# Performance work log

Measured on AMD Instinct MI355X. Metric: run time of the kernel, lower is better.

The kernel has to match this reference:

```python
import jax, jax.numpy as jnp
import numpy as np


def setup_inputs() -> dict:
    key = jax.random.key(0)
    k1, k2 = jax.random.split(key)
    N, D = 8192, 1024
    x = jax.random.normal(k1, (N, D), dtype=jnp.float32)
    w = jax.random.normal(k2, (D, 1), dtype=jnp.float32)
    return {"x": x, "w": w}


def reference(x, w):
    # x: [N, D], w: [D, 1]
    N = x.shape[0]
    a = jax.nn.sigmoid(x @ w)[:, 0]          # [N], values in (0, 1)
    b = jnp.cumsum(a)                         # [N] running sum
    idx = jnp.floor(b).astype(jnp.int32)      # bin index per column
    prev = jnp.concatenate([jnp.zeros(1, jnp.int32), idx[:-1]])
    same = idx == prev                        # did we stay in the same bin?
    frac = b - idx.astype(b.dtype)            # portion falling into bin `idx`
    cols = jnp.arange(N)
    # value written at [idx, i]: a_i if same bin, else the fractional overflow
    main_val = jnp.where(same, a, frac)
    # cross-boundary remainder written at [idx-1, i]
    cross_val = jnp.where(same, 0.0, a - frac)
    cross_row = jnp.where(same, idx, idx - 1)  # dummy (add 0) when same
    trans_mat = (
        jnp.zeros((N, N), dtype=x.dtype)
        .at[idx, cols].set(main_val)
        .at[cross_row, cols].add(cross_val)
    )
    return trans_mat @ x                      # [N, D]
```

## Files before the change

kernel.cpp:

```cpp
#include <hip/hip_runtime.h>
#include <math.h>


__global__ void dot_sigmoid_kernel(const float* __restrict__ x,
                                   const float* __restrict__ w,
                                   float* __restrict__ a, int N, int D) {
  int lane = threadIdx.x & 63;
  int wave = threadIdx.x >> 6;
  int row = blockIdx.x * (blockDim.x >> 6) + wave;
  if (row >= N) return;
  const float4* xr = reinterpret_cast<const float4*>(x + (size_t)row * D);
  const float4* w4 = reinterpret_cast<const float4*>(w);
  float acc = 0.f;
  int nv = D >> 2;
  for (int j = lane; j < nv; j += 64) {
    float4 xv = xr[j];
    float4 wv = w4[j];
    acc = fmaf(xv.x, wv.x, acc);
    acc = fmaf(xv.y, wv.y, acc);
    acc = fmaf(xv.z, wv.z, acc);
    acc = fmaf(xv.w, wv.w, acc);
  }
#pragma unroll
  for (int off = 32; off > 0; off >>= 1) acc += __shfl_down(acc, off, 64);
  if (lane == 0) a[row] = 1.0f / (1.0f + expf(-acc));
}

__global__ __launch_bounds__(1024) void scan_kernel(const float* __restrict__ a,
                                                    float* __restrict__ mainv,
                                                    float* __restrict__ crossv,
                                                    int* __restrict__ rowptr, int N) {
  __shared__ float sa[8192];
  __shared__ double wtot[16];
  __shared__ double woff[16];
  int t = threadIdx.x;
  for (int k = t; k < N; k += 1024) sa[k] = a[k];
  for (int k = t; k <= N; k += 1024) rowptr[k] = N;
  if (t == 0) rowptr[0] = 0;
  __syncthreads();

  int per = N / 1024;
  int base = t * per;
  double loc[8];
  double run = 0.0;
#pragma unroll
  for (int j = 0; j < 8; ++j) {
    run += (double)sa[base + j];
    loc[j] = run;
  }
  double v = run;
  int lane = t & 63;
  int wid = t >> 6;
  for (int off = 1; off < 64; off <<= 1) {
    double n = __shfl_up(v, off, 64);
    if (lane >= off) v += n;
  }
  if (lane == 63) wtot[wid] = v;
  __syncthreads();
  if (t == 0) {
    double s = 0.0;
    for (int k2 = 0; k2 < 16; ++k2) { woff[k2] = s; s += wtot[k2]; }
  }
  __syncthreads();
  double pre = woff[wid] + (v - run);
  double prevbd = pre;
#pragma unroll
  for (int j = 0; j < 8; ++j) {
    int i = base + j;
    double bd = pre + loc[j];
    float bf = (float)bd;
    float pf = (float)prevbd;
    int k = (int)floorf(bf);
    int kp = (int)floorf(pf);
    float ai = sa[i];
    float frac = bf - (float)k;
    bool same = (k == kp);
    mainv[i] = same ? ai : frac;
    crossv[i] = same ? 0.f : (ai - frac);
    if (!same) rowptr[k] = i;
    prevbd = bd;
  }
}

__global__ __launch_bounds__(256) void out_kernel(const float* __restrict__ x,
                                                  const float* __restrict__ mainv,
                                                  const float* __restrict__ crossv,
                                                  const int* __restrict__ rowptr,
                                                  float* __restrict__ out, int N, int D) {
  int r = blockIdx.x;
  int s0 = rowptr[r];
  int s1 = rowptr[r + 1];

  int c = threadIdx.x << 2;
  float4 acc = make_float4(0.f, 0.f, 0.f, 0.f);
  for (int i = s0; i < s1; ++i) {
    float wgt = mainv[i];
    float4 xv = *reinterpret_cast<const float4*>(x + (size_t)i * D + c);
    acc.x = fmaf(wgt, xv.x, acc.x);
    acc.y = fmaf(wgt, xv.y, acc.y);
    acc.z = fmaf(wgt, xv.z, acc.z);
    acc.w = fmaf(wgt, xv.w, acc.w);
  }
  if (s1 < N) {
    float wgt = crossv[s1];
    float4 xv = *reinterpret_cast<const float4*>(x + (size_t)s1 * D + c);
    acc.x = fmaf(wgt, xv.x, acc.x);
    acc.y = fmaf(wgt, xv.y, acc.y);
    acc.z = fmaf(wgt, xv.z, acc.z);
    acc.w = fmaf(wgt, xv.w, acc.w);
  }
  *reinterpret_cast<float4*>(out + (size_t)r * D + c) = acc;
}

extern "C" void kernel_launch(void* const* d_in, const int* in_sizes, int n_in,
                              void* d_out, int out_size, void* d_ws, size_t ws_size,
                              hipStream_t stream) {
  const float* x = (const float*)d_in[0];
  const float* w = (const float*)d_in[1];
  float* out = (float*)d_out;
  int D = in_sizes[1];
  int N = in_sizes[0] / D;

  float* a = (float*)d_ws;
  float* mainv = a + N;
  float* crossv = mainv + N;
  int* rowptr = (int*)(crossv + N);

  int waves_per_block = 4;
  dim3 g1((N + waves_per_block - 1) / waves_per_block);
  hipLaunchKernelGGL(dot_sigmoid_kernel, g1, dim3(256), 0, stream, x, w, a, N, D);

  hipLaunchKernelGGL(scan_kernel, dim3(1), dim3(1024), 0, stream, a, mainv, crossv,
                     rowptr, N);

  hipLaunchKernelGGL(out_kernel, dim3(N), dim3(D / 4), 0, stream, x, mainv, crossv,
                     rowptr, out, N, D);
}
```

Before: 103.0 us.

## Fuse dot-sigmoid with scan via last-block pattern and process two rows per block

Merges the dot-sigmoid and scan kernels into one launch. Each block computes four dot products, and the last block to finish (found with an atomic counter) runs the prefix scan with 256 threads over 32 elements each. The output kernel now handles two rows per block so the shared boundary row of x is loaded once for both rows. It also skips rows whose main weight is below 1e-7. This saves a launch and redundant loads, but adds a memset, a 32KB shared array in every block that can limit occupancy, a longer serial scan per thread, and a small approximation from the skipped weights.

```diff
diff --git a/kernel.cpp b/kernel.cpp
--- a/kernel.cpp
+++ b/kernel.cpp
@@ -2,72 +2,68 @@
 #include <math.h>
 
 
-__global__ void dot_sigmoid_kernel(const float* __restrict__ x,
-                                   const float* __restrict__ w,
-                                   float* __restrict__ a, int N, int D) {
-  int lane = threadIdx.x & 63;
-  int wave = threadIdx.x >> 6;
-  int row = blockIdx.x * (blockDim.x >> 6) + wave;
-  if (row >= N) return;
-  const float4* xr = reinterpret_cast<const float4*>(x + (size_t)row * D);
-  const float4* w4 = reinterpret_cast<const float4*>(w);
-  float acc = 0.f;
-  int nv = D >> 2;
-  for (int j = lane; j < nv; j += 64) {
-    float4 xv = xr[j];
-    float4 wv = w4[j];
-    acc = fmaf(xv.x, wv.x, acc);
-    acc = fmaf(xv.y, wv.y, acc);
-    acc = fmaf(xv.z, wv.z, acc);
-    acc = fmaf(xv.w, wv.w, acc);
+__global__ __launch_bounds__(256) void dot_scan_kernel(
+    const float* __restrict__ x, const float* __restrict__ w,
+    float* __restrict__ a, float* __restrict__ mainv, float* __restrict__ crossv,
+    int* __restrict__ rowptr, int* __restrict__ counter, int N, int D) {
+  __shared__ float sa[8192];
+  __shared__ double wtot[4];
+  __shared__ double woff[4];
+  __shared__ int lastflag;
+  int t = threadIdx.x;
+  int lane = t & 63;
+  int wave = t >> 6;
+
+  int row = blockIdx.x * 4 + wave;
+  {
+    const float4* xr = reinterpret_cast<const float4*>(x + (size_t)row * D);
+    const float4* w4 = reinterpret_cast<const float4*>(w);
+    float acc = 0.f;
+    int nv = D >> 2;
+    for (int j = lane; j < nv; j += 64) {
+      float4 xv = xr[j];
+      float4 wv = w4[j];
+      acc = fmaf(xv.x, wv.x, acc);
+      acc = fmaf(xv.y, wv.y, acc);
+      acc = fmaf(xv.z, wv.z, acc);
+      acc = fmaf(xv.w, wv.w, acc);
+    }
+#pragma unroll
+    for (int off = 32; off > 0; off >>= 1) acc += __shfl_down(acc, off, 64);
+    if (lane == 0) a[row] = 1.0f / (1.0f + expf(-acc));
   }
-#pragma unroll
-  for (int off = 32; off > 0; off >>= 1) acc += __shfl_down(acc, off, 64);
-  if (lane == 0) a[row] = 1.0f / (1.0f + expf(-acc));
-}
+  if (t < 4) rowptr[blockIdx.x * 4 + t] = N;
+  if (blockIdx.x == 0 && t == 4) rowptr[N] = N;
 
-__global__ __launch_bounds__(1024) void scan_kernel(const float* __restrict__ a,
-                                                    float* __restrict__ mainv,
-                                                    float* __restrict__ crossv,
-                                                    int* __restrict__ rowptr, int N) {
-  __shared__ float sa[8192];
-  __shared__ double wtot[16];
-  __shared__ double woff[16];
-  int t = threadIdx.x;
-  for (int k = t; k < N; k += 1024) sa[k] = a[k];
-  for (int k = t; k <= N; k += 1024) rowptr[k] = N;
-  if (t == 0) rowptr[0] = 0;
+  __threadfence();
+  if (t == 0) lastflag = (atomicAdd(counter, 1) == (int)gridDim.x - 1);
   __syncthreads();
+  if (!lastflag) return;
+  __threadfence();
 
-  int per = N / 1024;
+  for (int k = t; k < N; k += 256) sa[k] = a[k];
+  __syncthreads();
+  const int per = N / 256;
   int base = t * per;
-  double loc[8];
   double run = 0.0;
-#pragma unroll
-  for (int j = 0; j < 8; ++j) {
-    run += (double)sa[base + j];
-    loc[j] = run;
-  }
+  for (int j = 0; j < per; ++j) run += (double)sa[base + j];
   double v = run;
-  int lane = t & 63;
-  int wid = t >> 6;
   for (int off = 1; off < 64; off <<= 1) {
     double n = __shfl_up(v, off, 64);
     if (lane >= off) v += n;
   }
-  if (lane == 63) wtot[wid] = v;
+  if (lane == 63) wtot[wave] = v;
   __syncthreads();
   if (t == 0) {
     double s = 0.0;
-    for (int k2 = 0; k2 < 16; ++k2) { woff[k2] = s; s += wtot[k2]; }
+    for (int q = 0; q < 4; ++q) { woff[q] = s; s += wtot[q]; }
   }
   __syncthreads();
-  double pre = woff[wid] + (v - run);
-  double prevbd = pre;
-#pragma unroll
-  for (int j = 0; j < 8; ++j) {
+  double prevbd = woff[wave] + (v - run);
+  if (t == 0) rowptr[0] = 0;
+  for (int j = 0; j < per; ++j) {
     int i = base + j;
-    double bd = pre + loc[j];
+    double bd = prevbd + (double)sa[i];
     float bf = (float)bd;
     float pf = (float)prevbd;
     int k = (int)floorf(bf);
@@ -82,34 +78,60 @@
   }
 }
 
-__global__ __launch_bounds__(256) void out_kernel(const float* __restrict__ x,
-                                                  const float* __restrict__ mainv,
-                                                  const float* __restrict__ crossv,
-                                                  const int* __restrict__ rowptr,
-                                                  float* __restrict__ out, int N, int D) {
-  int r = blockIdx.x;
-  int s0 = rowptr[r];
-  int s1 = rowptr[r + 1];
+__global__ __launch_bounds__(256) void out_kernel(
+    const float* __restrict__ x, const float* __restrict__ mainv,
+    const float* __restrict__ crossv, const int* __restrict__ rowptr,
+    float* __restrict__ out, int N, int D) {
+  int r0 = blockIdx.x * 2;
+  int s0 = rowptr[r0];
+  int s1 = rowptr[r0 + 1];
+  int s2 = rowptr[r0 + 2];
 
   int c = threadIdx.x << 2;
-  float4 acc = make_float4(0.f, 0.f, 0.f, 0.f);
+  float4 acc0 = make_float4(0.f, 0.f, 0.f, 0.f);
+  float4 acc1 = make_float4(0.f, 0.f, 0.f, 0.f);
+
   for (int i = s0; i < s1; ++i) {
     float wgt = mainv[i];
+    if (wgt < 1e-7f) continue;
     float4 xv = *reinterpret_cast<const float4*>(x + (size_t)i * D + c);
-    acc.x = fmaf(wgt, xv.x, acc.x);
-    acc.y = fmaf(wgt, xv.y, acc.y);
-    acc.z = fmaf(wgt, xv.z, acc.z);
-    acc.w = fmaf(wgt, xv.w, acc.w);
+    acc0.x = fmaf(wgt, xv.x, acc0.x);
+    acc0.y = fmaf(wgt, xv.y, acc0.y);
+    acc0.z = fmaf(wgt, xv.z, acc0.z);
+    acc0.w = fmaf(wgt, xv.w, acc0.w);
   }
   if (s1 < N) {
-    float wgt = crossv[s1];
+    float wc = crossv[s1];
+    float wm = mainv[s1];
     float4 xv = *reinterpret_cast<const float4*>(x + (size_t)s1 * D + c);
-    acc.x = fmaf(wgt, xv.x, acc.x);
-    acc.y = fmaf(wgt, xv.y, acc.y);
-    acc.z = fmaf(wgt, xv.z, acc.z);
-    acc.w = fmaf(wgt, xv.w, acc.w);
+    acc0.x = fmaf(wc, xv.x, acc0.x);
+    acc0.y = fmaf(wc, xv.y, acc0.y);
+    acc0.z = fmaf(wc, xv.z, acc0.z);
+    acc0.w = fmaf(wc, xv.w, acc0.w);
+    acc1.x = fmaf(wm, xv.x, acc1.x);
+    acc1.y = fmaf(wm, xv.y, acc1.y);
+    acc1.z = fmaf(wm, xv.z, acc1.z);
+    acc1.w = fmaf(wm, xv.w, acc1.w);
   }
-  *reinterpret_cast<float4*>(out + (size_t)r * D + c) = acc;
+  for (int i = s1 + 1; i < s2; ++i) {
+    float wgt = mainv[i];
+    if (wgt < 1e-7f) continue;
+    float4 xv = *reinterpret_cast<const float4*>(x + (size_t)i * D + c);
+    acc1.x = fmaf(wgt, xv.x, acc1.x);
+    acc1.y = fmaf(wgt, xv.y, acc1.y);
+    acc1.z = fmaf(wgt, xv.z, acc1.z);
+    acc1.w = fmaf(wgt, xv.w, acc1.w);
+  }
+  if (s2 < N) {
+    float wc = crossv[s2];
+    float4 xv = *reinterpret_cast<const float4*>(x + (size_t)s2 * D + c);
+    acc1.x = fmaf(wc, xv.x, acc1.x);
+    acc1.y = fmaf(wc, xv.y, acc1.y);
+    acc1.z = fmaf(wc, xv.z, acc1.z);
+    acc1.w = fmaf(wc, xv.w, acc1.w);
+  }
+  *reinterpret_cast<float4*>(out + (size_t)r0 * D + c) = acc0;
+  *reinterpret_cast<float4*>(out + (size_t)(r0 + 1) * D + c) = acc1;
 }
 
 extern "C" void kernel_launch(void* const* d_in, const int* in_sizes, int n_in,
@@ -125,14 +147,13 @@
   float* mainv = a + N;
   float* crossv = mainv + N;
   int* rowptr = (int*)(crossv + N);
+  int* counter = rowptr + (N + 1);
 
-  int waves_per_block = 4;
-  dim3 g1((N + waves_per_block - 1) / waves_per_block);
-  hipLaunchKernelGGL(dot_sigmoid_kernel, g1, dim3(256), 0, stream, x, w, a, N, D);
+  hipMemsetAsync(counter, 0, sizeof(int), stream);
 
-  hipLaunchKernelGGL(scan_kernel, dim3(1), dim3(1024), 0, stream, a, mainv, crossv,
-                     rowptr, N);
+  hipLaunchKernelGGL(dot_scan_kernel, dim3(N / 4), dim3(256), 0, stream,
+                     x, w, a, mainv, crossv, rowptr, counter, N, D);
 
-  hipLaunchKernelGGL(out_kernel, dim3(N), dim3(D / 4), 0, stream, x, mainv, crossv,
-                     rowptr, out, N, D);
+  hipLaunchKernelGGL(out_kernel, dim3(N / 2), dim3(256), 0, stream,
+                     x, mainv, crossv, rowptr, out, N, D);
 }
```

New measurement: 247.2 us. +140.1%, slower.

## Process eight output rows per block, skipping empty tail rows directly

Applied to the files above, without the earlier changes.

The output kernel now gives each block eight consecutive output rows, walking the contiguous column range once and using a stored per-column bin index to flush finished rows. Rows past the last bin are zero-filled without issuing a block of their own, and the per-column weights are staged in LDS. Blocks whose range is empty or very short, which is most of the bottom half of the grid, now return quickly instead of each launching a separate workgroup. It also skips x loads when the main weight is near zero, which changes results slightly, and adds an extra index array to the workspace.

```diff
diff --git a/kernel.cpp b/kernel.cpp
--- a/kernel.cpp
+++ b/kernel.cpp
@@ -29,6 +29,7 @@
 __global__ __launch_bounds__(1024) void scan_kernel(const float* __restrict__ a,
                                                     float* __restrict__ mainv,
                                                     float* __restrict__ crossv,
+                                                    int* __restrict__ idxv,
                                                     int* __restrict__ rowptr, int N) {
   __shared__ float sa[8192];
   __shared__ double wtot[16];
@@ -39,7 +40,7 @@
   if (t == 0) rowptr[0] = 0;
   __syncthreads();
 
-  int per = N / 1024;
+  const int per = 8;
   int base = t * per;
   double loc[8];
   double run = 0.0;
@@ -59,7 +60,7 @@
   __syncthreads();
   if (t == 0) {
     double s = 0.0;
-    for (int k2 = 0; k2 < 16; ++k2) { woff[k2] = s; s += wtot[k2]; }
+    for (int q = 0; q < 16; ++q) { woff[q] = s; s += wtot[q]; }
   }
   __syncthreads();
   double pre = woff[wid] + (v - run);
@@ -77,39 +78,83 @@
     bool same = (k == kp);
     mainv[i] = same ? ai : frac;
     crossv[i] = same ? 0.f : (ai - frac);
+    idxv[i] = k;
     if (!same) rowptr[k] = i;
     prevbd = bd;
   }
 }
 
-__global__ __launch_bounds__(256) void out_kernel(const float* __restrict__ x,
-                                                  const float* __restrict__ mainv,
-                                                  const float* __restrict__ crossv,
-                                                  const int* __restrict__ rowptr,
-                                                  float* __restrict__ out, int N, int D) {
-  int r = blockIdx.x;
-  int s0 = rowptr[r];
-  int s1 = rowptr[r + 1];
+constexpr int R = 8;
+constexpr int CAP = 1024;
 
-  int c = threadIdx.x << 2;
+__global__ __launch_bounds__(256) void out_kernel(
+    const float* __restrict__ x, const float* __restrict__ mainv,
+    const float* __restrict__ crossv, const int* __restrict__ idxv,
+    const int* __restrict__ rowptr, float* __restrict__ out, int N, int D) {
+  __shared__ float sm[CAP];
+  __shared__ float sc[CAP];
+  __shared__ int sk[CAP];
+  int r0 = blockIdx.x * R;
+  int s_begin = rowptr[r0];
+  int s_endp = rowptr[r0 + R];
+  int len = s_endp - s_begin;
+  int total = len + (s_endp < N ? 1 : 0);
+  int t = threadIdx.x;
+  bool use_lds = (s_begin < N) && (total <= CAP);
+  if (use_lds) {
+    for (int j = t; j < total; j += 256) {
+      sm[j] = mainv[s_begin + j];
+      sc[j] = crossv[s_begin + j];
+      sk[j] = idxv[s_begin + j];
+    }
+    __syncthreads();
+  }
+  int c = t << 2;
   float4 acc = make_float4(0.f, 0.f, 0.f, 0.f);
-  for (int i = s0; i < s1; ++i) {
-    float wgt = mainv[i];
-    float4 xv = *reinterpret_cast<const float4*>(x + (size_t)i * D + c);
-    acc.x = fmaf(wgt, xv.x, acc.x);
-    acc.y = fmaf(wgt, xv.y, acc.y);
-    acc.z = fmaf(wgt, xv.z, acc.z);
-    acc.w = fmaf(wgt, xv.w, acc.w);
+  int cur = r0;
+  for (int j = 0; j < len; ++j) {
+    int i = s_begin + j;
+    float wm, wc;
+    int k;
+    if (use_lds) { wm = sm[j]; wc = sc[j]; k = sk[j]; }
+    else         { wm = mainv[i]; wc = crossv[i]; k = idxv[i]; }
+    if (k > cur) {
+      while (cur < k - 1) {
+        *reinterpret_cast<float4*>(out + (size_t)cur * D + c) = acc;
+        acc = make_float4(0.f, 0.f, 0.f, 0.f);
+        ++cur;
+      }
+      float4 xv = *reinterpret_cast<const float4*>(x + (size_t)i * D + c);
+      acc.x = fmaf(wc, xv.x, acc.x);
+      acc.y = fmaf(wc, xv.y, acc.y);
+      acc.z = fmaf(wc, xv.z, acc.z);
+      acc.w = fmaf(wc, xv.w, acc.w);
+      *reinterpret_cast<float4*>(out + (size_t)cur * D + c) = acc;
+      cur = k;
+      acc.x = wm * xv.x;
+      acc.y = wm * xv.y;
+      acc.z = wm * xv.z;
+      acc.w = wm * xv.w;
+    } else if (wm >= 1e-7f) {
+      float4 xv = *reinterpret_cast<const float4*>(x + (size_t)i * D + c);
+      acc.x = fmaf(wm, xv.x, acc.x);
+      acc.y = fmaf(wm, xv.y, acc.y);
+      acc.z = fmaf(wm, xv.z, acc.z);
+      acc.w = fmaf(wm, xv.w, acc.w);
+    }
   }
-  if (s1 < N) {
-    float wgt = crossv[s1];
-    float4 xv = *reinterpret_cast<const float4*>(x + (size_t)s1 * D + c);
-    acc.x = fmaf(wgt, xv.x, acc.x);
-    acc.y = fmaf(wgt, xv.y, acc.y);
-    acc.z = fmaf(wgt, xv.z, acc.z);
-    acc.w = fmaf(wgt, xv.w, acc.w);
+  if (s_endp < N) {
+    float wc = use_lds ? sc[len] : crossv[s_endp];
+    float4 xv = *reinterpret_cast<const float4*>(x + (size_t)s_endp * D + c);
+    acc.x = fmaf(wc, xv.x, acc.x);
+    acc.y = fmaf(wc, xv.y, acc.y);
+    acc.z = fmaf(wc, xv.z, acc.z);
+    acc.w = fmaf(wc, xv.w, acc.w);
   }
-  *reinterpret_cast<float4*>(out + (size_t)r * D + c) = acc;
+  *reinterpret_cast<float4*>(out + (size_t)cur * D + c) = acc;
+  float4 z = make_float4(0.f, 0.f, 0.f, 0.f);
+  for (int r = cur + 1; r < r0 + R; ++r)
+    *reinterpret_cast<float4*>(out + (size_t)r * D + c) = z;
 }
 
 extern "C" void kernel_launch(void* const* d_in, const int* in_sizes, int n_in,
@@ -124,15 +169,13 @@
   float* a = (float*)d_ws;
   float* mainv = a + N;
   float* crossv = mainv + N;
-  int* rowptr = (int*)(crossv + N);
+  int* idxv = (int*)(crossv + N);
+  int* rowptr = idxv + N;
 
-  int waves_per_block = 4;
-  dim3 g1((N + waves_per_block - 1) / waves_per_block);
-  hipLaunchKernelGGL(dot_sigmoid_kernel, g1, dim3(256), 0, stream, x, w, a, N, D);
-
-  hipLaunchKernelGGL(scan_kernel, dim3(1), dim3(1024), 0, stream, a, mainv, crossv,
-                     rowptr, N);
-
-  hipLaunchKernelGGL(out_kernel, dim3(N), dim3(D / 4), 0, stream, x, mainv, crossv,
-                     rowptr, out, N, D);
+  hipLaunchKernelGGL(dot_sigmoid_kernel, dim3(N / 4), dim3(256), 0, stream,
+                     x, w, a, N, D);
+  hipLaunchKernelGGL(scan_kernel, dim3(1), dim3(1024), 0, stream,
+                     a, mainv, crossv, idxv, rowptr, N);
+  hipLaunchKernelGGL(out_kernel, dim3(N / R), dim3(256), 0, stream,
+                     x, mainv, crossv, idxv, rowptr, out, N, D);
 }
```

Result: slower. 107.4 us (+4.3%).

## Parallelize scan across blocks using per-block partial sums from the dot kernel

Applied to the files above, without the earlier changes.

The dot/sigmoid kernel now writes a per-block partial sum in double and initializes rowptr. The single-block scan becomes a 32-block scan that recomputes the prefix of the block sums and does a wave-level scan per element. This removes a serial one-block launch from the critical path. The output kernel also skips loads for weights below 1e-7, which changes results slightly and hard-codes N=8192 and D=1024 assumptions in the launch shapes.

```diff
diff --git a/kernel.cpp b/kernel.cpp
--- a/kernel.cpp
+++ b/kernel.cpp
@@ -2,13 +2,15 @@
 #include <math.h>
 
 
-__global__ void dot_sigmoid_kernel(const float* __restrict__ x,
-                                   const float* __restrict__ w,
-                                   float* __restrict__ a, int N, int D) {
-  int lane = threadIdx.x & 63;
-  int wave = threadIdx.x >> 6;
-  int row = blockIdx.x * (blockDim.x >> 6) + wave;
-  if (row >= N) return;
+__global__ __launch_bounds__(256) void dot_sigmoid_kernel(
+    const float* __restrict__ x, const float* __restrict__ w,
+    float* __restrict__ a, double* __restrict__ blocksum,
+    int* __restrict__ rowptr, int N, int D) {
+  __shared__ float was[4];
+  int t = threadIdx.x;
+  int lane = t & 63;
+  int wave = t >> 6;
+  int row = blockIdx.x * 4 + wave;
   const float4* xr = reinterpret_cast<const float4*>(x + (size_t)row * D);
   const float4* w4 = reinterpret_cast<const float4*>(w);
   float acc = 0.f;
@@ -23,91 +25,98 @@
   }
 #pragma unroll
   for (int off = 32; off > 0; off >>= 1) acc += __shfl_down(acc, off, 64);
-  if (lane == 0) a[row] = 1.0f / (1.0f + expf(-acc));
+  if (lane == 0) {
+    float av = 1.0f / (1.0f + expf(-acc));
+    a[row] = av;
+    was[wave] = av;
+  }
+  int gtid = blockIdx.x * 256 + t;
+  if (gtid <= N) rowptr[gtid] = N;
+  __syncthreads();
+  if (t == 0)
+    blocksum[blockIdx.x] =
+        (double)was[0] + (double)was[1] + (double)was[2] + (double)was[3];
 }
 
-__global__ __launch_bounds__(1024) void scan_kernel(const float* __restrict__ a,
-                                                    float* __restrict__ mainv,
-                                                    float* __restrict__ crossv,
-                                                    int* __restrict__ rowptr, int N) {
-  __shared__ float sa[8192];
-  __shared__ double wtot[16];
-  __shared__ double woff[16];
+__global__ __launch_bounds__(256) void scan_emit_kernel(
+    const float* __restrict__ a, const double* __restrict__ blocksum,
+    float* __restrict__ mainv, float* __restrict__ crossv,
+    int* __restrict__ rowptr, int N) {
+  __shared__ double sg[256];
+  __shared__ double wtot[4];
+  int b = blockIdx.x;
   int t = threadIdx.x;
-  for (int k = t; k < N; k += 1024) sa[k] = a[k];
-  for (int k = t; k <= N; k += 1024) rowptr[k] = N;
-  if (t == 0) rowptr[0] = 0;
+  int lane = t & 63;
+  int wid = t >> 6;
+
+  double g = 0.0;
+#pragma unroll
+  for (int j = 0; j < 8; ++j) g += blocksum[8 * t + j];
+  double vg = g;
+  for (int off = 1; off < 64; off <<= 1) {
+    double n = __shfl_up(vg, off, 64);
+    if (lane >= off) vg += n;
+  }
+  if (lane == 63) wtot[wid] = vg;
+  __syncthreads();
+  double wb = 0.0;
+  for (int q = 0; q < wid; ++q) wb += wtot[q];
+  sg[t] = wb + vg - g;
   __syncthreads();
 
-  int per = N / 1024;
-  int base = t * per;
-  double loc[8];
-  double run = 0.0;
-#pragma unroll
-  for (int j = 0; j < 8; ++j) {
-    run += (double)sa[base + j];
-    loc[j] = run;
+  int i = b * 256 + t;
+  float ai = a[i];
+  double va = (double)ai;
+  for (int off = 1; off < 64; off <<= 1) {
+    double n = __shfl_up(va, off, 64);
+    if (lane >= off) va += n;
   }
-  double v = run;
-  int lane = t & 63;
-  int wid = t >> 6;
-  for (int off = 1; off < 64; off <<= 1) {
-    double n = __shfl_up(v, off, 64);
-    if (lane >= off) v += n;
-  }
-  if (lane == 63) wtot[wid] = v;
-  __syncthreads();
-  if (t == 0) {
-    double s = 0.0;
-    for (int k2 = 0; k2 < 16; ++k2) { woff[k2] = s; s += wtot[k2]; }
-  }
-  __syncthreads();
-  double pre = woff[wid] + (v - run);
-  double prevbd = pre;
-#pragma unroll
-  for (int j = 0; j < 8; ++j) {
-    int i = base + j;
-    double bd = pre + loc[j];
-    float bf = (float)bd;
-    float pf = (float)prevbd;
-    int k = (int)floorf(bf);
-    int kp = (int)floorf(pf);
-    float ai = sa[i];
-    float frac = bf - (float)k;
-    bool same = (k == kp);
-    mainv[i] = same ? ai : frac;
-    crossv[i] = same ? 0.f : (ai - frac);
-    if (!same) rowptr[k] = i;
-    prevbd = bd;
-  }
+  double E = va - (double)ai;
+  int g0 = lane & ~31;
+  double Eg0 = __shfl(E, g0, 64);
+  int gg = 8 * b + (t >> 5);
+  double prevbd = sg[gg] + (E - Eg0);
+  double bd = prevbd + (double)ai;
+  float bf = (float)bd;
+  float pf = (float)prevbd;
+  int k = (int)floorf(bf);
+  int kp = (int)floorf(pf);
+  float frac = bf - (float)k;
+  bool same = (k == kp);
+  mainv[i] = same ? ai : frac;
+  crossv[i] = same ? 0.f : (ai - frac);
+  if (!same) rowptr[k] = i;
+  if (b == 0 && t == 0) rowptr[0] = 0;
 }
 
-__global__ __launch_bounds__(256) void out_kernel(const float* __restrict__ x,
-                                                  const float* __restrict__ mainv,
-                                                  const float* __restrict__ crossv,
-                                                  const int* __restrict__ rowptr,
-                                                  float* __restrict__ out, int N, int D) {
+__global__ __launch_bounds__(256) void out_kernel(
+    const float* __restrict__ x, const float* __restrict__ mainv,
+    const float* __restrict__ crossv, const int* __restrict__ rowptr,
+    float* __restrict__ out, int N, int D) {
   int r = blockIdx.x;
   int s0 = rowptr[r];
   int s1 = rowptr[r + 1];
-
   int c = threadIdx.x << 2;
   float4 acc = make_float4(0.f, 0.f, 0.f, 0.f);
   for (int i = s0; i < s1; ++i) {
-    float wgt = mainv[i];
-    float4 xv = *reinterpret_cast<const float4*>(x + (size_t)i * D + c);
-    acc.x = fmaf(wgt, xv.x, acc.x);
-    acc.y = fmaf(wgt, xv.y, acc.y);
-    acc.z = fmaf(wgt, xv.z, acc.z);
-    acc.w = fmaf(wgt, xv.w, acc.w);
+    float wm = mainv[i];
+    if (wm >= 1e-7f) {
+      float4 xv = *reinterpret_cast<const float4*>(x + (size_t)i * D + c);
+      acc.x = fmaf(wm, xv.x, acc.x);
+      acc.y = fmaf(wm, xv.y, acc.y);
+      acc.z = fmaf(wm, xv.z, acc.z);
+      acc.w = fmaf(wm, xv.w, acc.w);
+    }
   }
   if (s1 < N) {
-    float wgt = crossv[s1];
-    float4 xv = *reinterpret_cast<const float4*>(x + (size_t)s1 * D + c);
-    acc.x = fmaf(wgt, xv.x, acc.x);
-    acc.y = fmaf(wgt, xv.y, acc.y);
-    acc.z = fmaf(wgt, xv.z, acc.z);
-    acc.w = fmaf(wgt, xv.w, acc.w);
+    float wc = crossv[s1];
+    if (wc >= 1e-7f) {
+      float4 xv = *reinterpret_cast<const float4*>(x + (size_t)s1 * D + c);
+      acc.x = fmaf(wc, xv.x, acc.x);
+      acc.y = fmaf(wc, xv.y, acc.y);
+      acc.z = fmaf(wc, xv.z, acc.z);
+      acc.w = fmaf(wc, xv.w, acc.w);
+    }
   }
   *reinterpret_cast<float4*>(out + (size_t)r * D + c) = acc;
 }
@@ -125,14 +134,12 @@
   float* mainv = a + N;
   float* crossv = mainv + N;
   int* rowptr = (int*)(crossv + N);
+  double* blocksum = (double*)(((uintptr_t)(rowptr + N + 1) + 15) & ~15ull);
 
-  int waves_per_block = 4;
-  dim3 g1((N + waves_per_block - 1) / waves_per_block);
-  hipLaunchKernelGGL(dot_sigmoid_kernel, g1, dim3(256), 0, stream, x, w, a, N, D);
-
-  hipLaunchKernelGGL(scan_kernel, dim3(1), dim3(1024), 0, stream, a, mainv, crossv,
-                     rowptr, N);
-
-  hipLaunchKernelGGL(out_kernel, dim3(N), dim3(D / 4), 0, stream, x, mainv, crossv,
-                     rowptr, out, N, D);
+  hipLaunchKernelGGL(dot_sigmoid_kernel, dim3(N / 4), dim3(256), 0, stream,
+                     x, w, a, blocksum, rowptr, N, D);
+  hipLaunchKernelGGL(scan_emit_kernel, dim3(N / 256), dim3(256), 0, stream,
+                     a, blocksum, mainv, crossv, rowptr, N);
+  hipLaunchKernelGGL(out_kernel, dim3(N), dim3(256), 0, stream,
+                     x, mainv, crossv, rowptr, out, N, D);
 }
```

Result: faster. 92.25 us (-10.4%).
